# Optimization experiments

Hardware: AMD Instinct MI355X
Metric: run time of the kernel (lower is better)

Reference implementation:

```python
import jax, jax.numpy as jnp
import numpy as np

B, S, D = 2, 2048, 2048
H, KV, HD = 32, 8, 64
REP = H // KV


def rotate_half(t):
    t1, t2 = t[..., : t.shape[-1] // 2], t[..., t.shape[-1] // 2 :]
    return jnp.concatenate((-t2, t1), axis=-1)


def setup_inputs() -> dict:
    key = jax.random.key(0)
    kx, kq, kk, kv, ko = jax.random.split(key, 5)
    x = jax.random.normal(kx, (B, S, D), dtype=jnp.float32) * 0.02
    # RoPE tables: shape [S, HD//2]; forward concatenates [cos, cos] to reach HD
    inv_freq = 1.0 / (10000.0 ** (np.arange(0, HD, 2, dtype=np.float32) / HD))
    freqs = np.outer(np.arange(S, dtype=np.float32), inv_freq)
    cos = jnp.asarray(np.cos(freqs), dtype=jnp.float32)
    sin = jnp.asarray(np.sin(freqs), dtype=jnp.float32)
    # causal additive mask [1,1,S,S]
    causal = np.tril(np.ones((S, S), dtype=bool))
    mask = jnp.asarray(np.where(causal, 0.0, -1e9).astype(np.float32))[None, None]
    s = 0.02
    wq = jax.random.normal(kq, (H * HD, D), dtype=jnp.float32) * s
    wk = jax.random.normal(kk, (KV * HD, D), dtype=jnp.float32) * s
    wv = jax.random.normal(kv, (KV * HD, D), dtype=jnp.float32) * s
    wo = jax.random.normal(ko, (D, H * HD), dtype=jnp.float32) * s
    return {"x": x, "cos": cos, "sin": sin, "mask": mask,
            "wq": wq, "wk": wk, "wv": wv, "wo": wo}


def reference(x, cos, sin, mask, wq, wk, wv, wo):
    b, s, d = x.shape
    # QKV projections (Linear with bias=False: x @ W^T)
    q = jnp.einsum("bsd,ed->bse", x, wq).reshape(b, s, H, HD)
    k = jnp.einsum("bsd,ed->bse", x, wk).reshape(b, s, KV, HD)
    v = jnp.einsum("bsd,ed->bse", x, wv).reshape(b, s, KV, HD)
    # RoPE: cos/sin [S, HD//2] -> [1, S, 1, HD]
    cc = jnp.concatenate([cos[:s], cos[:s]], axis=-1)[None, :, None, :]
    ss = jnp.concatenate([sin[:s], sin[:s]], axis=-1)[None, :, None, :]
    q = q * cc + rotate_half(q) * ss
    k = k * cc + rotate_half(k) * ss
    # GQA: group q heads by kv head (implicit broadcast instead of repeat_kv)
    q = q.transpose(0, 2, 1, 3).reshape(b, KV, REP, s, HD)  # [B,KV,REP,S,HD]
    k = k.transpose(0, 2, 1, 3)                              # [B,KV,S,HD]
    v = v.transpose(0, 2, 1, 3)                              # [B,KV,S,HD]
    scores = jnp.einsum("bkrqd,bksd->bkrqs", q, k) / np.sqrt(HD)
    scores = scores + mask[:, :, None, :, :]  # broadcast over rep dim
    probs = jax.nn.softmax(scores.astype(jnp.float32), axis=-1).astype(q.dtype)
    out = jnp.einsum("bkrqs,bksd->bkrqd", probs, v)
    out = out.transpose(0, 3, 1, 2, 4).reshape(b, s, H * HD)  # [B,S,H*HD]
    return jnp.einsum("bse,de->bsd", out, wo)
```

## Files before the change

kernel.cpp:

```cpp
#include <hip/hip_runtime.h>
#include <stdint.h>

#define DEV __device__ __forceinline__

typedef __bf16 bf16;
typedef __bf16 bf16x8 __attribute__((ext_vector_type(8)));
typedef __bf16 bf16x4v __attribute__((ext_vector_type(4)));
typedef float f32x4 __attribute__((ext_vector_type(4)));
typedef float f32x16 __attribute__((ext_vector_type(16)));
typedef int int2v __attribute__((ext_vector_type(2)));

constexpr int Bb = 2, Ss = 2048, Dd = 2048, Hh = 32, KVh = 8, HDd = 64;
constexpr int Mm = Bb * Ss;
constexpr int EQ = Hh * HDd;
constexpr int EKV = KVh * HDd;
constexpr int Ee = EQ + 2 * EKV;

DEV void gload16(const void* g, void* l) {
  __builtin_amdgcn_global_load_lds((const __attribute__((address_space(1))) uint32_t*)g,
                                   (__attribute__((address_space(3))) uint32_t*)l, 16, 0, 0);
}

DEV float exp2_fast(float x) {
  float r;
  asm("v_exp_f32 %0, %1\n\ts_nop 0" : "=v"(r) : "v"(x));
  return r;
}
DEV uint32_t cvtpk(float lo, float hi) {
  uint32_t w;
  asm("v_cvt_pk_bf16_f32 %0, %1, %2" : "=v"(w) : "v"(lo), "v"(hi));
  return w;
}
DEV int2v pswap(uint32_t a, uint32_t b) {
  return __builtin_amdgcn_permlane32_swap((int)a, (int)b, false, false);
}
DEV float fu(uint32_t u) { union { uint32_t u; float f; } c; c.u = u; return c.f; }
DEV uint32_t uf(float f) { union { float f; uint32_t u; } c; c.f = f; return c.u; }

__global__ void cvt_kernel(const float* __restrict__ x, const float* __restrict__ wq,
                           const float* __restrict__ wk, const float* __restrict__ wv,
                           const float* __restrict__ wo,
                           bf16* __restrict__ xb, bf16* __restrict__ wqkvb,
                           bf16* __restrict__ wob) {
  const long NX = (long)Mm * Dd;
  const long NQ = (long)EQ * Dd;
  const long NK = (long)EKV * Dd;
  const long NO = (long)Dd * EQ;
  const long total4 = (NX + NQ + 2 * NK + NO) / 4;
  for (long i = (long)blockIdx.x * blockDim.x + threadIdx.x; i < total4;
       i += (long)gridDim.x * blockDim.x) {
    long e = i * 4;
    const float* src; bf16* dst;
    if (e < NX)                { src = x + e;                       dst = xb + e; }
    else if (e < NX + NQ)      { long o = e - NX;                   src = wq + o; dst = wqkvb + o; }
    else if (e < NX + NQ + NK) { long o = e - NX - NQ;              src = wk + o; dst = wqkvb + NQ + o; }
    else if (e < NX + NQ + 2*NK){ long o = e - NX - NQ - NK;        src = wv + o; dst = wqkvb + NQ + NK + o; }
    else                       { long o = e - NX - NQ - 2*NK;       src = wo + o; dst = wob + o; }
    float4 v = *(const float4*)src;
    bf16x4v b;
    b.x = (bf16)v.x; b.y = (bf16)v.y; b.z = (bf16)v.z; b.w = (bf16)v.w;
    *(bf16x4v*)dst = b;
  }
}

template <int BN, bool OUT_BF16>
__global__ __launch_bounds__(512, 1)
void gemm_bt(const bf16* __restrict__ A, const bf16* __restrict__ Bt,
             float* __restrict__ Cf, bf16* __restrict__ Cb,
             int Mn, int Nn, int Kn) {
  constexpr int NJ = BN / 64;
  constexpr int RB = BN / 4;
  __shared__ __align__(16) bf16 As[2][256 * 64];
  __shared__ __align__(16) bf16 Bs[2][BN * 64];
  const int tid = threadIdx.x, wid = tid >> 6, lane = tid & 63;
  const int g = lane >> 4, c = lane & 15;
  const int wm = wid >> 2, wn = wid & 3;

  const int nbj = Nn / BN;
  const int nwg = (Mn >> 8) * nbj;
  const int cpx = nwg >> 3;
  const int swz = ((int)blockIdx.x % 8) * cpx + (int)blockIdx.x / 8;
  const int bi = swz / nbj, bj = swz % nbj;
  const long arow0 = (long)bi * 256, brow0 = (long)bj * BN;

  const int srow = tid >> 3, schk = tid & 7;
  const int cs = schk ^ (srow & 7);

  f32x4 acc[8][NJ] = {};

#pragma unroll
  for (int it = 0; it < 4; ++it) {
    gload16(A + (arow0 + it * 64 + srow) * Kn + cs * 8,
            (char*)&As[0][0] + it * 8192 + tid * 16);
    if (tid < RB * 8)
      gload16(Bt + (brow0 + it * RB + srow) * Kn + cs * 8,
              (char*)&Bs[0][0] + it * RB * 128 + tid * 16);
  }
  __syncthreads();

  const int NT = Kn >> 6;
  for (int kt = 0; kt < NT; ++kt) {
    const char* pa = (const char*)&As[kt & 1][0];
    const char* pb = (const char*)&Bs[kt & 1][0];
    char* na = (char*)&As[(kt + 1) & 1][0];
    char* nb = (char*)&Bs[(kt + 1) & 1][0];
    const bool more = (kt + 1 < NT);
    bf16x8 bfr[NJ][2];

#pragma unroll
    for (int p = 0; p < 4; ++p) {
      bf16x8 af[2][2];
#pragma unroll
      for (int i2 = 0; i2 < 2; ++i2)
#pragma unroll
        for (int ks = 0; ks < 2; ++ks) {
          int r = wm * 128 + (2 * p + i2) * 16 + c;
          af[i2][ks] = *(const bf16x8*)(pa + r * 128 + (((ks * 4 + g) ^ (r & 7)) << 4));
        }
      if (p == 0) {
#pragma unroll
        for (int j = 0; j < NJ; ++j)
#pragma unroll
          for (int ks = 0; ks < 2; ++ks) {
            int r = wn * RB + j * 16 + c;
            bfr[j][ks] = *(const bf16x8*)(pb + r * 128 + (((ks * 4 + g) ^ (r & 7)) << 4));
          }
      }
      if (more) {
        gload16(A + (arow0 + p * 64 + srow) * Kn + (kt + 1) * 64 + cs * 8,
                na + p * 8192 + tid * 16);
        if (tid < RB * 8)
          gload16(Bt + (brow0 + p * RB + srow) * Kn + (kt + 1) * 64 + cs * 8,
                  nb + p * RB * 128 + tid * 16);
      }
      __builtin_amdgcn_s_barrier();
      asm volatile("s_waitcnt lgkmcnt(0)" ::: "memory");
      __builtin_amdgcn_s_setprio(1);
#pragma unroll
      for (int i2 = 0; i2 < 2; ++i2)
#pragma unroll
        for (int j = 0; j < NJ; ++j)
#pragma unroll
          for (int ks = 0; ks < 2; ++ks)
            acc[2 * p + i2][j] =
                __builtin_amdgcn_mfma_f32_16x16x32_bf16(af[i2][ks], bfr[j][ks],
                                                        acc[2 * p + i2][j], 0, 0, 0);
      __builtin_amdgcn_s_setprio(0);
      if (p < 3) __builtin_amdgcn_s_barrier();
    }
    __syncthreads();
  }

#pragma unroll
  for (int i = 0; i < 8; ++i)
#pragma unroll
    for (int j = 0; j < NJ; ++j)
#pragma unroll
      for (int r = 0; r < 4; ++r) {
        long row = arow0 + wm * 128 + i * 16 + 4 * g + r;
        long col = brow0 + wn * RB + j * 16 + c;
        if (OUT_BF16) Cb[row * Nn + col] = (bf16)acc[i][j][r];
        else          Cf[row * Nn + col] = acc[i][j][r];
      }
}

__global__ void rope_qk_kernel(const bf16* __restrict__ qkv, const float* __restrict__ cosT,
                               const float* __restrict__ sinT, bf16* __restrict__ qout,
                               bf16* __restrict__ kout) {
  int tid = blockIdx.x * blockDim.x + threadIdx.x;
  const int NQT = Mm * Hh * 32;
  if (tid < NQT) {
    int d = tid & 31;
    int h = (tid >> 5) & (Hh - 1);
    int m = tid >> 10;
    int s = m & (Ss - 1), b = m >> 11;
    float lo = (float)qkv[(long)m * Ee + h * 64 + d];
    float hi = (float)qkv[(long)m * Ee + h * 64 + d + 32];
    float cs = cosT[s * 32 + d], sn = sinT[s * 32 + d];
    long base = (((long)(b * Hh + h)) * Ss + s) * 64;
    qout[base + d]      = (bf16)(lo * cs - hi * sn);
    qout[base + d + 32] = (bf16)(hi * cs + lo * sn);
  } else {
    int t = tid - NQT;
    if (t >= Mm * KVh * 32) return;
    int d = t & 31;
    int h = (t >> 5) & (KVh - 1);
    int m = t >> 8;
    int s = m & (Ss - 1), b = m >> 11;
    float lo = (float)qkv[(long)m * Ee + EQ + h * 64 + d];
    float hi = (float)qkv[(long)m * Ee + EQ + h * 64 + d + 32];
    float cs = cosT[s * 32 + d], sn = sinT[s * 32 + d];
    long base = (((long)(b * KVh + h)) * Ss + s) * 64;
    kout[base + d]      = (bf16)(lo * cs - hi * sn);
    kout[base + d + 32] = (bf16)(hi * cs + lo * sn);
  }
}

__global__ void vtrans_kernel(const bf16* __restrict__ qkv, bf16* __restrict__ vtb) {
  __shared__ __align__(16) unsigned short tile[64][72];
  int blk = blockIdx.x;
  int st = blk & 31, kvh = (blk >> 5) & 7, b = blk >> 8;
  int s0 = st * 64;
  int t = threadIdx.x;
#pragma unroll
  for (int rep = 0; rep < 2; ++rep) {
    int idx = t + rep * 256;
    int r = idx >> 3, cb = idx & 7;
    const bf16* src = qkv + ((long)(b * Ss + s0 + r)) * Ee + EQ + EKV + kvh * 64 + cb * 8;
    *(uint4*)&tile[r][cb * 8] = *(const uint4*)src;
  }
  __syncthreads();
#pragma unroll
  for (int rep = 0; rep < 2; ++rep) {
    int idx = t + rep * 256;
    int dd = idx >> 3, scb = idx & 7;
    union { unsigned short u[8]; uint4 v; } pk;
#pragma unroll
    for (int j = 0; j < 8; ++j) pk.u[j] = tile[scb * 8 + j][dd];
    long dst = ((long)((b * KVh + kvh) * 64 + dd)) * Ss + s0 + scb * 8;
    *(uint4*)&vtb[dst] = pk.v;
  }
}

__global__ __launch_bounds__(512)
void attn_kernel(const bf16* __restrict__ q, const bf16* __restrict__ k,
                 const bf16* __restrict__ vt, bf16* __restrict__ o) {
  __shared__ __align__(16) bf16 Kt[2][64 * 64];
  __shared__ __align__(16) bf16 Vt[2][64 * 64];
  constexpr float SCL = 0.18033688f;
  constexpr float THR = 44.36f;

  const int tid = threadIdx.x, qw = tid >> 6, lane = tid & 63;
  const int ql = lane & 31, hi = lane >> 5;
  const int qt = 7 - (int)(blockIdx.x >> 6);
  const int bh = blockIdx.x & 63;
  const int b = bh >> 5, h = bh & 31;
  const int kvh = h >> 2;
  const int q0 = qt * 256;
  const int qw_q0 = q0 + qw * 32;

  const bf16* kbase = k + ((long)(b * KVh + kvh)) * Ss * 64;
  const bf16* vbase = vt + ((long)(b * KVh + kvh)) * 64 * Ss;

  const int srow = tid >> 3, scb = tid & 7;
  const int scbs = scb ^ (srow & 7);
  const int sdst = tid * 16;

  bf16x8 qf[4];
  {
    const bf16* qrow = q + (((long)bh) * Ss + q0 + qw * 32 + ql) * 64 + 8 * hi;
#pragma unroll
    for (int ks = 0; ks < 4; ++ks) qf[ks] = *(const bf16x8*)(qrow + 16 * ks);
  }

  gload16(kbase + (long)srow * 64 + scbs * 8, (char*)&Kt[0][0] + sdst);
  gload16(vbase + (long)srow * Ss + scbs * 8, (char*)&Vt[0][0] + sdst);
  __syncthreads();

  f32x16 Oacc0 = {}, Oacc1 = {};
  float m_run = -1e30f, l_run = 0.f;
  const int qa = qw_q0 + ql;
  const int nt = 4 * qt + 4;
  const int tdiag = qw_q0 >> 6;

  int cur = 0;
  for (int t = 0; t < nt; ++t) {
    if (t + 1 < nt) {
      int nb = cur ^ 1;
      gload16(kbase + ((long)(t + 1) * 64 + srow) * 64 + scbs * 8, (char*)&Kt[nb][0] + sdst);
      gload16(vbase + (long)srow * Ss + (t + 1) * 64 + scbs * 8, (char*)&Vt[nb][0] + sdst);
    }

    if (64 * t < qw_q0 + 32) {
      f32x16 s0 = {}, s1 = {};
      const char* kt = (const char*)&Kt[cur][0];
#pragma unroll
      for (int ks = 0; ks < 4; ++ks) {
        int chk = ((2 * ks + hi) ^ (ql & 7)) << 4;
        bf16x8 kf0 = *(const bf16x8*)(kt + ql * 128 + chk);
        bf16x8 kf1 = *(const bf16x8*)(kt + (32 + ql) * 128 + chk);
        s0 = __builtin_amdgcn_mfma_f32_32x32x16_bf16(kf0, qf[ks], s0, 0, 0, 0);
        s1 = __builtin_amdgcn_mfma_f32_32x32x16_bf16(kf1, qf[ks], s1, 0, 0, 0);
      }

      if (t == tdiag) {
#pragma unroll
        for (int r = 0; r < 16; ++r) {
          int kv0 = t * 64 + (r & 3) + 8 * (r >> 2) + 4 * hi;
          if (kv0 > qa)      s0[r] = -1e30f;
          if (kv0 + 32 > qa) s1[r] = -1e30f;
        }
      }

      float mx[16];
#pragma unroll
      for (int r = 0; r < 16; ++r) mx[r] = fmaxf(s0[r], s1[r]);
#pragma unroll
      for (int st2 = 8; st2 > 0; st2 >>= 1)
#pragma unroll
        for (int r = 0; r < 8; ++r)
          if (r < st2) mx[r] = fmaxf(mx[r], mx[r + st2]);
      float pm;
      {
        int2v rr = pswap(uf(mx[0]), uf(mx[0]));
        pm = fmaxf(fu(rr.x), fu(rr.y));
      }

      if (__any(pm > m_run + THR)) {
        float mn = fmaxf(m_run, pm);
        float corr = exp2_fast((m_run - mn) * SCL);
#pragma unroll
        for (int r = 0; r < 16; ++r) {
          float co = __shfl(corr, (r & 3) + 8 * (r >> 2) + 4 * hi);
          Oacc0[r] *= co; Oacc1[r] *= co;
        }
        l_run *= corr;
        m_run = mn;
      }

      const float mcs = m_run * SCL;
#pragma unroll
      for (int r = 0; r < 16; ++r) {
        s0[r] = exp2_fast(fmaf(s0[r], SCL, -mcs));
        s1[r] = exp2_fast(fmaf(s1[r], SCL, -mcs));
      }
      float sm[16];
#pragma unroll
      for (int r = 0; r < 16; ++r) sm[r] = s0[r] + s1[r];
#pragma unroll
      for (int st2 = 8; st2 > 0; st2 >>= 1)
#pragma unroll
        for (int r = 0; r < 8; ++r)
          if (r < st2) sm[r] += sm[r + st2];
      {
        int2v rr = pswap(uf(sm[0]), uf(sm[0]));
        l_run += fu(rr.x) + fu(rr.y);
      }

      const char* vtb0 = (const char*)&Vt[cur][0];
#pragma unroll
      for (int ks = 0; ks < 4; ++ks) {
        uint32_t pk01, pk23, pk45, pk67;
        if (ks < 2) {
          const int rb = (ks & 1) * 8;
          pk01 = cvtpk(s0[rb + 0], s0[rb + 1]);
          pk23 = cvtpk(s0[rb + 2], s0[rb + 3]);
          pk45 = cvtpk(s0[rb + 4], s0[rb + 5]);
          pk67 = cvtpk(s0[rb + 6], s0[rb + 7]);
        } else {
          const int rb = (ks & 1) * 8;
          pk01 = cvtpk(s1[rb + 0], s1[rb + 1]);
          pk23 = cvtpk(s1[rb + 2], s1[rb + 3]);
          pk45 = cvtpk(s1[rb + 4], s1[rb + 5]);
          pk67 = cvtpk(s1[rb + 6], s1[rb + 7]);
        }
        int2v w02 = pswap(pk01, pk45);
        int2v w13 = pswap(pk23, pk67);
        union { uint32_t u[4]; bf16x8 v; } pa;
        pa.u[0] = (uint32_t)w02.x; pa.u[1] = (uint32_t)w13.x;
        pa.u[2] = (uint32_t)w02.y; pa.u[3] = (uint32_t)w13.y;

        int chk = ((2 * ks + hi) ^ (ql & 7)) << 4;
        bf16x8 vf0 = *(const bf16x8*)(vtb0 + ql * 128 + chk);
        bf16x8 vf1 = *(const bf16x8*)(vtb0 + (32 + ql) * 128 + chk);
        Oacc0 = __builtin_amdgcn_mfma_f32_32x32x16_bf16(pa.v, vf0, Oacc0, 0, 0, 0);
        Oacc1 = __builtin_amdgcn_mfma_f32_32x32x16_bf16(pa.v, vf1, Oacc1, 0, 0, 0);
      }
    }

    __syncthreads();
    cur ^= 1;
  }

  float linv = 1.0f / l_run;
#pragma unroll
  for (int r = 0; r < 16; ++r) {
    int qrow = (r & 3) + 8 * (r >> 2) + 4 * hi;
    float li = __shfl(linv, qrow);
    long orow = (long)b * Ss + q0 + 32 * qw + qrow;
    o[orow * EQ + h * 64 + ql]      = (bf16)(Oacc0[r] * li);
    o[orow * EQ + h * 64 + 32 + ql] = (bf16)(Oacc1[r] * li);
  }
}

extern "C" void kernel_launch(void* const* d_in, const int* in_sizes, int n_in,
                              void* d_out, int out_size, void* d_ws, size_t ws_size,
                              hipStream_t stream) {
  const float* x    = (const float*)d_in[0];
  const float* cosT = (const float*)d_in[1];
  const float* sinT = (const float*)d_in[2];
  const float* wq   = (const float*)d_in[4];
  const float* wk   = (const float*)d_in[5];
  const float* wv   = (const float*)d_in[6];
  const float* wo   = (const float*)d_in[7];

  if (ws_size < 104857600u) return;

  char* ws = (char*)d_ws;
  bf16* xb    = (bf16*)(ws + 0);
  bf16* wqkvb = (bf16*)(ws + 16777216);
  bf16* wob   = (bf16*)(ws + 29360128);
  bf16* qkvb  = (bf16*)(ws + 37748736);
  bf16* qb    = (bf16*)(ws + 62914560);
  bf16* kb    = (bf16*)(ws + 79691776);
  bf16* vtb   = (bf16*)(ws + 83886080);
  bf16* attnb = (bf16*)(ws + 88080384);
  float* outp = (float*)d_out;

  cvt_kernel<<<dim3(2048), dim3(256), 0, stream>>>(x, wq, wk, wv, wo, xb, wqkvb, wob);
  gemm_bt<192, true><<<dim3((Mm / 256) * (Ee / 192)), dim3(512), 0, stream>>>(
      xb, wqkvb, (float*)nullptr, qkvb, Mm, Ee, Dd);
  rope_qk_kernel<<<dim3((Mm * (Hh + KVh) * 32) / 256), dim3(256), 0, stream>>>(
      qkvb, cosT, sinT, qb, kb);
  vtrans_kernel<<<dim3(Bb * KVh * 32), dim3(256), 0, stream>>>(qkvb, vtb);
  attn_kernel<<<dim3(512), dim3(512), 0, stream>>>(qb, kb, vtb, attnb);
  gemm_bt<128, false><<<dim3((Mm / 256) * (EQ / 128)), dim3(512), 0, stream>>>(
      attnb, wob, outp, (bf16*)nullptr, Mm, EQ, EQ);
}
```

Before: 192.7 us.

## Fuse Q RoPE into attention, double K/V tile per barrier, reorder q-tiles

Applies RoPE to Q inside the attention kernel, reading raw Q straight from the QKV buffer, so the separate Q rope pass and its intermediate buffer go away and the rope kernel handles only K. The attention loop now loads two 64-wide K/V tiles per stage (doubling LDS use) so there are half as many barriers per KV sweep. The q-tile scheduling order is also changed so the first half of blocks are heavy and the second half light. The cost is more LDS per block, which can lower occupancy, and extra register pressure from the in-kernel rope.

```diff
diff --git a/kernel.cpp b/kernel.cpp
--- a/kernel.cpp
+++ b/kernel.cpp
@@ -164,36 +164,20 @@
       }
 }
 
-__global__ void rope_qk_kernel(const bf16* __restrict__ qkv, const float* __restrict__ cosT,
-                               const float* __restrict__ sinT, bf16* __restrict__ qout,
-                               bf16* __restrict__ kout) {
+__global__ void rope_k_kernel(const bf16* __restrict__ qkv, const float* __restrict__ cosT,
+                              const float* __restrict__ sinT, bf16* __restrict__ kout) {
   int tid = blockIdx.x * blockDim.x + threadIdx.x;
-  const int NQT = Mm * Hh * 32;
-  if (tid < NQT) {
-    int d = tid & 31;
-    int h = (tid >> 5) & (Hh - 1);
-    int m = tid >> 10;
-    int s = m & (Ss - 1), b = m >> 11;
-    float lo = (float)qkv[(long)m * Ee + h * 64 + d];
-    float hi = (float)qkv[(long)m * Ee + h * 64 + d + 32];
-    float cs = cosT[s * 32 + d], sn = sinT[s * 32 + d];
-    long base = (((long)(b * Hh + h)) * Ss + s) * 64;
-    qout[base + d]      = (bf16)(lo * cs - hi * sn);
-    qout[base + d + 32] = (bf16)(hi * cs + lo * sn);
-  } else {
-    int t = tid - NQT;
-    if (t >= Mm * KVh * 32) return;
-    int d = t & 31;
-    int h = (t >> 5) & (KVh - 1);
-    int m = t >> 8;
-    int s = m & (Ss - 1), b = m >> 11;
-    float lo = (float)qkv[(long)m * Ee + EQ + h * 64 + d];
-    float hi = (float)qkv[(long)m * Ee + EQ + h * 64 + d + 32];
-    float cs = cosT[s * 32 + d], sn = sinT[s * 32 + d];
-    long base = (((long)(b * KVh + h)) * Ss + s) * 64;
-    kout[base + d]      = (bf16)(lo * cs - hi * sn);
-    kout[base + d + 32] = (bf16)(hi * cs + lo * sn);
-  }
+  int d = tid & 31;
+  int h = (tid >> 5) & (KVh - 1);
+  int m = tid >> 8;
+  if (m >= Mm) return;
+  int s = m & (Ss - 1), b = m >> 11;
+  float lo = (float)qkv[(long)m * Ee + EQ + h * 64 + d];
+  float hi = (float)qkv[(long)m * Ee + EQ + h * 64 + d + 32];
+  float cs = cosT[s * 32 + d], sn = sinT[s * 32 + d];
+  long base = (((long)(b * KVh + h)) * Ss + s) * 64;
+  kout[base + d]      = (bf16)(lo * cs - hi * sn);
+  kout[base + d + 32] = (bf16)(hi * cs + lo * sn);
 }
 
 __global__ void vtrans_kernel(const bf16* __restrict__ qkv, bf16* __restrict__ vtb) {
@@ -223,16 +207,18 @@
 }
 
 __global__ __launch_bounds__(512)
-void attn_kernel(const bf16* __restrict__ q, const bf16* __restrict__ k,
+void attn_kernel(const bf16* __restrict__ qkv, const float* __restrict__ cosT,
+                 const float* __restrict__ sinT, const bf16* __restrict__ k,
                  const bf16* __restrict__ vt, bf16* __restrict__ o) {
-  __shared__ __align__(16) bf16 Kt[2][64 * 64];
-  __shared__ __align__(16) bf16 Vt[2][64 * 64];
+  __shared__ __align__(16) bf16 Kt[2][2][64 * 64];
+  __shared__ __align__(16) bf16 Vt[2][2][64 * 64];
   constexpr float SCL = 0.18033688f;
   constexpr float THR = 44.36f;
 
   const int tid = threadIdx.x, qw = tid >> 6, lane = tid & 63;
   const int ql = lane & 31, hi = lane >> 5;
-  const int qt = 7 - (int)(blockIdx.x >> 6);
+  const int g6 = (int)(blockIdx.x >> 6);
+  const int qt = (g6 < 4) ? (7 - g6) : (g6 - 4);
   const int bh = blockIdx.x & 63;
   const int b = bh >> 5, h = bh & 31;
   const int kvh = h >> 2;
@@ -248,123 +234,153 @@
 
   bf16x8 qf[4];
   {
-    const bf16* qrow = q + (((long)bh) * Ss + q0 + qw * 32 + ql) * 64 + 8 * hi;
-#pragma unroll
-    for (int ks = 0; ks < 4; ++ks) qf[ks] = *(const bf16x8*)(qrow + 16 * ks);
-  }
-
-  gload16(kbase + (long)srow * 64 + scbs * 8, (char*)&Kt[0][0] + sdst);
-  gload16(vbase + (long)srow * Ss + scbs * 8, (char*)&Vt[0][0] + sdst);
+    const int s_row = q0 + qw * 32 + ql;
+    const bf16* qrow = qkv + ((long)(b * Ss + s_row)) * Ee + h * 64 + 8 * hi;
+    bf16x8 qraw[4];
+#pragma unroll
+    for (int ks = 0; ks < 4; ++ks) qraw[ks] = *(const bf16x8*)(qrow + 16 * ks);
+    float cs8[2][8], sn8[2][8];
+#pragma unroll
+    for (int ks2 = 0; ks2 < 2; ++ks2) {
+      const float* cp = cosT + s_row * 32 + 16 * ks2 + 8 * hi;
+      const float* sp = sinT + s_row * 32 + 16 * ks2 + 8 * hi;
+      *(float4*)&cs8[ks2][0] = *(const float4*)cp;
+      *(float4*)&cs8[ks2][4] = *(const float4*)(cp + 4);
+      *(float4*)&sn8[ks2][0] = *(const float4*)sp;
+      *(float4*)&sn8[ks2][4] = *(const float4*)(sp + 4);
+    }
+#pragma unroll
+    for (int ks2 = 0; ks2 < 2; ++ks2)
+#pragma unroll
+      for (int j = 0; j < 8; ++j) {
+        float lo = (float)qraw[ks2][j], hv = (float)qraw[ks2 + 2][j];
+        qf[ks2][j]     = (bf16)(lo * cs8[ks2][j] - hv * sn8[ks2][j]);
+        qf[ks2 + 2][j] = (bf16)(hv * cs8[ks2][j] + lo * sn8[ks2][j]);
+      }
+  }
+
+  gload16(kbase + (long)srow * 64 + scbs * 8, (char*)&Kt[0][0][0] + sdst);
+  gload16(kbase + ((long)64 + srow) * 64 + scbs * 8, (char*)&Kt[0][1][0] + sdst);
+  gload16(vbase + (long)srow * Ss + scbs * 8, (char*)&Vt[0][0][0] + sdst);
+  gload16(vbase + (long)srow * Ss + 64 + scbs * 8, (char*)&Vt[0][1][0] + sdst);
   __syncthreads();
 
   f32x16 Oacc0 = {}, Oacc1 = {};
   float m_run = -1e30f, l_run = 0.f;
   const int qa = qw_q0 + ql;
   const int nt = 4 * qt + 4;
+  const int ntp = nt >> 1;
   const int tdiag = qw_q0 >> 6;
 
   int cur = 0;
-  for (int t = 0; t < nt; ++t) {
-    if (t + 1 < nt) {
+  for (int pp = 0; pp < ntp; ++pp) {
+    if (pp + 1 < ntp) {
       int nb = cur ^ 1;
-      gload16(kbase + ((long)(t + 1) * 64 + srow) * 64 + scbs * 8, (char*)&Kt[nb][0] + sdst);
-      gload16(vbase + (long)srow * Ss + (t + 1) * 64 + scbs * 8, (char*)&Vt[nb][0] + sdst);
+      long t0 = (long)(2 * pp + 2) * 64;
+      gload16(kbase + (t0 + srow) * 64 + scbs * 8, (char*)&Kt[nb][0][0] + sdst);
+      gload16(kbase + (t0 + 64 + srow) * 64 + scbs * 8, (char*)&Kt[nb][1][0] + sdst);
+      gload16(vbase + (long)srow * Ss + t0 + scbs * 8, (char*)&Vt[nb][0][0] + sdst);
+      gload16(vbase + (long)srow * Ss + t0 + 64 + scbs * 8, (char*)&Vt[nb][1][0] + sdst);
     }
 
-    if (64 * t < qw_q0 + 32) {
-      f32x16 s0 = {}, s1 = {};
-      const char* kt = (const char*)&Kt[cur][0];
-#pragma unroll
-      for (int ks = 0; ks < 4; ++ks) {
-        int chk = ((2 * ks + hi) ^ (ql & 7)) << 4;
-        bf16x8 kf0 = *(const bf16x8*)(kt + ql * 128 + chk);
-        bf16x8 kf1 = *(const bf16x8*)(kt + (32 + ql) * 128 + chk);
-        s0 = __builtin_amdgcn_mfma_f32_32x32x16_bf16(kf0, qf[ks], s0, 0, 0, 0);
-        s1 = __builtin_amdgcn_mfma_f32_32x32x16_bf16(kf1, qf[ks], s1, 0, 0, 0);
-      }
-
-      if (t == tdiag) {
+#pragma unroll
+    for (int half = 0; half < 2; ++half) {
+      const int t = 2 * pp + half;
+      if (64 * t < qw_q0 + 32) {
+        f32x16 s0 = {}, s1 = {};
+        const char* kt = (const char*)&Kt[cur][half][0];
+#pragma unroll
+        for (int ks = 0; ks < 4; ++ks) {
+          int chk = ((2 * ks + hi) ^ (ql & 7)) << 4;
+          bf16x8 kf0 = *(const bf16x8*)(kt + ql * 128 + chk);
+          bf16x8 kf1 = *(const bf16x8*)(kt + (32 + ql) * 128 + chk);
+          s0 = __builtin_amdgcn_mfma_f32_32x32x16_bf16(kf0, qf[ks], s0, 0, 0, 0);
+          s1 = __builtin_amdgcn_mfma_f32_32x32x16_bf16(kf1, qf[ks], s1, 0, 0, 0);
+        }
+
+        if (t == tdiag) {
+#pragma unroll
+          for (int r = 0; r < 16; ++r) {
+            int kv0 = t * 64 + (r & 3) + 8 * (r >> 2) + 4 * hi;
+            if (kv0 > qa)      s0[r] = -1e30f;
+            if (kv0 + 32 > qa) s1[r] = -1e30f;
+          }
+        }
+
+        float mx[16];
+#pragma unroll
+        for (int r = 0; r < 16; ++r) mx[r] = fmaxf(s0[r], s1[r]);
+#pragma unroll
+        for (int st2 = 8; st2 > 0; st2 >>= 1)
+#pragma unroll
+          for (int r = 0; r < 8; ++r)
+            if (r < st2) mx[r] = fmaxf(mx[r], mx[r + st2]);
+        float pm;
+        {
+          int2v rr = pswap(uf(mx[0]), uf(mx[0]));
+          pm = fmaxf(fu(rr.x), fu(rr.y));
+        }
+
+        if (__any(pm > m_run + THR)) {
+          float mn = fmaxf(m_run, pm);
+          float corr = exp2_fast((m_run - mn) * SCL);
+#pragma unroll
+          for (int r = 0; r < 16; ++r) {
+            float co = __shfl(corr, (r & 3) + 8 * (r >> 2) + 4 * hi);
+            Oacc0[r] *= co; Oacc1[r] *= co;
+          }
+          l_run *= corr;
+          m_run = mn;
+        }
+
+        const float mcs = m_run * SCL;
 #pragma unroll
         for (int r = 0; r < 16; ++r) {
-          int kv0 = t * 64 + (r & 3) + 8 * (r >> 2) + 4 * hi;
-          if (kv0 > qa)      s0[r] = -1e30f;
-          if (kv0 + 32 > qa) s1[r] = -1e30f;
-        }
-      }
-
-      float mx[16];
-#pragma unroll
-      for (int r = 0; r < 16; ++r) mx[r] = fmaxf(s0[r], s1[r]);
-#pragma unroll
-      for (int st2 = 8; st2 > 0; st2 >>= 1)
-#pragma unroll
-        for (int r = 0; r < 8; ++r)
-          if (r < st2) mx[r] = fmaxf(mx[r], mx[r + st2]);
-      float pm;
-      {
-        int2v rr = pswap(uf(mx[0]), uf(mx[0]));
-        pm = fmaxf(fu(rr.x), fu(rr.y));
-      }
-
-      if (__any(pm > m_run + THR)) {
-        float mn = fmaxf(m_run, pm);
-        float corr = exp2_fast((m_run - mn) * SCL);
-#pragma unroll
-        for (int r = 0; r < 16; ++r) {
-          float co = __shfl(corr, (r & 3) + 8 * (r >> 2) + 4 * hi);
-          Oacc0[r] *= co; Oacc1[r] *= co;
-        }
-        l_run *= corr;
-        m_run = mn;
-      }
-
-      const float mcs = m_run * SCL;
-#pragma unroll
-      for (int r = 0; r < 16; ++r) {
-        s0[r] = exp2_fast(fmaf(s0[r], SCL, -mcs));
-        s1[r] = exp2_fast(fmaf(s1[r], SCL, -mcs));
-      }
-      float sm[16];
-#pragma unroll
-      for (int r = 0; r < 16; ++r) sm[r] = s0[r] + s1[r];
-#pragma unroll
-      for (int st2 = 8; st2 > 0; st2 >>= 1)
-#pragma unroll
-        for (int r = 0; r < 8; ++r)
-          if (r < st2) sm[r] += sm[r + st2];
-      {
-        int2v rr = pswap(uf(sm[0]), uf(sm[0]));
-        l_run += fu(rr.x) + fu(rr.y);
-      }
-
-      const char* vtb0 = (const char*)&Vt[cur][0];
-#pragma unroll
-      for (int ks = 0; ks < 4; ++ks) {
-        uint32_t pk01, pk23, pk45, pk67;
-        if (ks < 2) {
-          const int rb = (ks & 1) * 8;
-          pk01 = cvtpk(s0[rb + 0], s0[rb + 1]);
-          pk23 = cvtpk(s0[rb + 2], s0[rb + 3]);
-          pk45 = cvtpk(s0[rb + 4], s0[rb + 5]);
-          pk67 = cvtpk(s0[rb + 6], s0[rb + 7]);
-        } else {
-          const int rb = (ks & 1) * 8;
-          pk01 = cvtpk(s1[rb + 0], s1[rb + 1]);
-          pk23 = cvtpk(s1[rb + 2], s1[rb + 3]);
-          pk45 = cvtpk(s1[rb + 4], s1[rb + 5]);
-          pk67 = cvtpk(s1[rb + 6], s1[rb + 7]);
-        }
-        int2v w02 = pswap(pk01, pk45);
-        int2v w13 = pswap(pk23, pk67);
-        union { uint32_t u[4]; bf16x8 v; } pa;
-        pa.u[0] = (uint32_t)w02.x; pa.u[1] = (uint32_t)w13.x;
-        pa.u[2] = (uint32_t)w02.y; pa.u[3] = (uint32_t)w13.y;
-
-        int chk = ((2 * ks + hi) ^ (ql & 7)) << 4;
-        bf16x8 vf0 = *(const bf16x8*)(vtb0 + ql * 128 + chk);
-        bf16x8 vf1 = *(const bf16x8*)(vtb0 + (32 + ql) * 128 + chk);
-        Oacc0 = __builtin_amdgcn_mfma_f32_32x32x16_bf16(pa.v, vf0, Oacc0, 0, 0, 0);
-        Oacc1 = __builtin_amdgcn_mfma_f32_32x32x16_bf16(pa.v, vf1, Oacc1, 0, 0, 0);
+          s0[r] = exp2_fast(fmaf(s0[r], SCL, -mcs));
+          s1[r] = exp2_fast(fmaf(s1[r], SCL, -mcs));
+        }
+        float sm[16];
+#pragma unroll
+        for (int r = 0; r < 16; ++r) sm[r] = s0[r] + s1[r];
+#pragma unroll
+        for (int st2 = 8; st2 > 0; st2 >>= 1)
+#pragma unroll
+          for (int r = 0; r < 8; ++r)
+            if (r < st2) sm[r] += sm[r + st2];
+        {
+          int2v rr = pswap(uf(sm[0]), uf(sm[0]));
+          l_run += fu(rr.x) + fu(rr.y);
+        }
+
+        const char* vtb0 = (const char*)&Vt[cur][half][0];
+#pragma unroll
+        for (int ks = 0; ks < 4; ++ks) {
+          uint32_t pk01, pk23, pk45, pk67;
+          if (ks < 2) {
+            const int rb = (ks & 1) * 8;
+            pk01 = cvtpk(s0[rb + 0], s0[rb + 1]);
+            pk23 = cvtpk(s0[rb + 2], s0[rb + 3]);
+            pk45 = cvtpk(s0[rb + 4], s0[rb + 5]);
+            pk67 = cvtpk(s0[rb + 6], s0[rb + 7]);
+          } else {
+            const int rb = (ks & 1) * 8;
+            pk01 = cvtpk(s1[rb + 0], s1[rb + 1]);
+            pk23 = cvtpk(s1[rb + 2], s1[rb + 3]);
+            pk45 = cvtpk(s1[rb + 4], s1[rb + 5]);
+            pk67 = cvtpk(s1[rb + 6], s1[rb + 7]);
+          }
+          int2v w02 = pswap(pk01, pk45);
+          int2v w13 = pswap(pk23, pk67);
+          union { uint32_t u[4]; bf16x8 v; } pa;
+          pa.u[0] = (uint32_t)w02.x; pa.u[1] = (uint32_t)w13.x;
+          pa.u[2] = (uint32_t)w02.y; pa.u[3] = (uint32_t)w13.y;
+
+          int chk = ((2 * ks + hi) ^ (ql & 7)) << 4;
+          bf16x8 vf0 = *(const bf16x8*)(vtb0 + ql * 128 + chk);
+          bf16x8 vf1 = *(const bf16x8*)(vtb0 + (32 + ql) * 128 + chk);
+          Oacc0 = __builtin_amdgcn_mfma_f32_32x32x16_bf16(pa.v, vf0, Oacc0, 0, 0, 0);
+          Oacc1 = __builtin_amdgcn_mfma_f32_32x32x16_bf16(pa.v, vf1, Oacc1, 0, 0, 0);
+        }
       }
     }
 
@@ -401,7 +417,6 @@
   bf16* wqkvb = (bf16*)(ws + 16777216);
   bf16* wob   = (bf16*)(ws + 29360128);
   bf16* qkvb  = (bf16*)(ws + 37748736);
-  bf16* qb    = (bf16*)(ws + 62914560);
   bf16* kb    = (bf16*)(ws + 79691776);
   bf16* vtb   = (bf16*)(ws + 83886080);
   bf16* attnb = (bf16*)(ws + 88080384);
@@ -410,10 +425,9 @@
   cvt_kernel<<<dim3(2048), dim3(256), 0, stream>>>(x, wq, wk, wv, wo, xb, wqkvb, wob);
   gemm_bt<192, true><<<dim3((Mm / 256) * (Ee / 192)), dim3(512), 0, stream>>>(
       xb, wqkvb, (float*)nullptr, qkvb, Mm, Ee, Dd);
-  rope_qk_kernel<<<dim3((Mm * (Hh + KVh) * 32) / 256), dim3(256), 0, stream>>>(
-      qkvb, cosT, sinT, qb, kb);
+  rope_k_kernel<<<dim3((Mm * KVh * 32) / 256), dim3(256), 0, stream>>>(qkvb, cosT, sinT, kb);
   vtrans_kernel<<<dim3(Bb * KVh * 32), dim3(256), 0, stream>>>(qkvb, vtb);
-  attn_kernel<<<dim3(512), dim3(512), 0, stream>>>(qb, kb, vtb, attnb);
+  attn_kernel<<<dim3(512), dim3(512), 0, stream>>>(qkvb, cosT, sinT, kb, vtb, attnb);
   gemm_bt<128, false><<<dim3((Mm / 256) * (EQ / 128)), dim3(512), 0, stream>>>(
       attnb, wob, outp, (bf16*)nullptr, Mm, EQ, EQ);
 }
```

Measured after the change: 184.5 us. 4.3% less time.
